# Kernel tuning notes

Measured on AMD Instinct MI355X. Metric: run time of the kernel, lower is better.

Reference implementation:

```python
import jax, jax.numpy as jnp
import numpy as np

EPS = 1e-5

def _conv1x1(x, w):
    # x: (B, Cin, N, K), w: (Cout, Cin) -> (B, Cout, N, K)
    return jnp.einsum('oc,bcnk->bonk', w, x)

def _bn2d(x, gamma, beta):
    # eval-mode BN with running_mean=0, running_var=1 (fresh init)
    scale = gamma / jnp.sqrt(1.0 + EPS)
    return x * scale[None, :, None, None] + beta[None, :, None, None]

def setup_inputs() -> dict:
    key = jax.random.key(0)
    ks = jax.random.split(key, 10)
    B, Cin, N, K = 8, 64, 1024, 32
    Cout, M = 64, 8
    Cin2 = 2 * Cin  # kernel_input='w_neighbor'
    features = jax.random.normal(ks[0], (B, Cin, N, K), dtype=jnp.float32)
    points_xyz = jax.random.normal(ks[1], (B, 3, N, K), dtype=jnp.float32)
    # ScoreNet convs: mlp_channels [7,16,16,16,M]; first 3 have BN (no bias), last has bias
    w1 = jax.random.normal(ks[2], (16, 7), dtype=jnp.float32) * (2.0 / 7) ** 0.5
    w2 = jax.random.normal(ks[3], (16, 16), dtype=jnp.float32) * (2.0 / 16) ** 0.5
    w3 = jax.random.normal(ks[4], (16, 16), dtype=jnp.float32) * (2.0 / 16) ** 0.5
    w4 = jax.random.normal(ks[5], (M, 16), dtype=jnp.float32) * (2.0 / 16) ** 0.5
    b4 = jnp.zeros((M,), dtype=jnp.float32)
    g1 = jnp.ones((16,), jnp.float32); be1 = jnp.zeros((16,), jnp.float32)
    g2 = jnp.ones((16,), jnp.float32); be2 = jnp.zeros((16,), jnp.float32)
    g3 = jnp.ones((16,), jnp.float32); be3 = jnp.zeros((16,), jnp.float32)
    # weight bank: kaiming_normal on (M, 2Cin, Cout) -> stored as (2Cin, M, Cout)
    wb = jax.random.normal(ks[6], (Cin2, M, Cout), dtype=jnp.float32) * (2.0 / Cin2) ** 0.5
    bn_g = jnp.ones((Cout,), jnp.float32); bn_b = jnp.zeros((Cout,), jnp.float32)
    return dict(features=features, points_xyz=points_xyz,
                w1=w1, g1=g1, be1=be1, w2=w2, g2=g2, be2=be2,
                w3=w3, g3=g3, be3=be3, w4=w4, b4=b4,
                weight_bank=wb, bn_g=bn_g, bn_b=bn_b)

def reference(features, points_xyz, w1, g1, be1, w2, g2, be2, w3, g3, be3,
              w4, b4, weight_bank, bn_g, bn_b):
    B, Cin, N, K = features.shape
    M = weight_bank.shape[1]
    # kernel_input = 'w_neighbor': concat(feat - center, feat) -> (B, 2Cin, N, K)
    center_f = features[..., :1]
    feat = jnp.concatenate([features - center_f, features], axis=1)
    # scorenet input = 'w_neighbor_dist': (center_xyz, xyz_diff, dist) -> (B, 7, N, K)
    center_xyz = jnp.broadcast_to(points_xyz[..., :1], points_xyz.shape)
    xyz_diff = points_xyz - center_xyz
    dist = jnp.sqrt(jnp.sum(xyz_diff * xyz_diff, axis=1, keepdims=True))
    xyz_feats = jnp.concatenate([center_xyz, xyz_diff, dist], axis=1)
    h = jax.nn.relu(_bn2d(_conv1x1(xyz_feats, w1), g1, be1))
    h = jax.nn.relu(_bn2d(_conv1x1(h, w2), g2, be2))
    h = jax.nn.relu(_bn2d(_conv1x1(h, w3), g3, be3))
    s = _conv1x1(h, w4) + b4[None, :, None, None]  # (B, M, N, K)
    scores = jax.nn.softmax(s, axis=1)
    scores = jnp.transpose(scores, (0, 2, 3, 1))  # (B, N, K, M)
    # matmul with weight bank then score-weighted sum over kernels, fused via einsum
    # original: (B,N,K,2Cin)@(2Cin,M*Cout) -> (B,N,K,M,Cout); sum_m scores * . -> (B,N,K,Cout)
    new_features = jnp.einsum('bcnk,cmo,bnkm->bonk', feat, weight_bank, scores)
    # BN2d (eval, fresh stats) + ReLU
    new_features = jax.nn.relu(_bn2d(new_features, bn_g, bn_b))
    return new_features
```

## Files before the change

kernel.cpp:

```cpp
#include <hip/hip_runtime.h>
#include <hip/hip_bf16.h>

typedef _Float16 f16;
typedef __attribute__((ext_vector_type(2))) _Float16 f16x2;
typedef __attribute__((ext_vector_type(8))) _Float16 f16x8;
typedef __attribute__((ext_vector_type(16))) float f32x16;

#define BNSCL 0.9999950000375f

__global__ __launch_bounds__(256) void k_scores(
    const float* __restrict__ xyz,
    const float* __restrict__ w1, const float* __restrict__ g1, const float* __restrict__ be1,
    const float* __restrict__ w2, const float* __restrict__ g2, const float* __restrict__ be2,
    const float* __restrict__ w3, const float* __restrict__ g3, const float* __restrict__ be3,
    const float* __restrict__ w4, const float* __restrict__ b4,
    const float* __restrict__ wb, f16* __restrict__ wbtA,
    f16* __restrict__ scores)
{
    __shared__ float lw[856];
    const int tid = threadIdx.x;

    if (blockIdx.x < 256) {
        int idx = blockIdx.x * 256 + tid;
        int j    = idx & 7;
        int lane = (idx >> 3) & 63;
        int ks   = (idx >> 9) & 63;
        int ot   = idx >> 15;
        int cp   = ks * 2 + (lane >> 5);
        int o    = ot * 32 + (lane & 31);
        wbtA[idx] = (f16)wb[(cp * 8 + j) * 64 + o];
    }

    if (tid < 112) lw[tid] = w1[tid];
    lw[112 + tid] = w2[tid];
    lw[368 + tid] = w3[tid];
    if (tid < 128) lw[624 + tid] = w4[tid];
    if (tid < 8)   lw[752 + tid] = b4[tid];
    if (tid < 16) {
        lw[760 + tid] = g1[tid] * BNSCL;  lw[776 + tid] = be1[tid];
        lw[792 + tid] = g2[tid] * BNSCL;  lw[808 + tid] = be2[tid];
        lw[824 + tid] = g3[tid] * BNSCL;  lw[840 + tid] = be3[tid];
    }
    __syncthreads();

    float in7[2][7], h1[2][16], h2[2][16], s[2][8];

#pragma unroll
    for (int q = 0; q < 2; ++q) {
        int g = blockIdx.x * 512 + q * 256 + tid;
        int b = g >> 15;
        int p = g & 32767;
        int pc = p & ~31;
        const float* xb = xyz + (size_t)b * 98304;
        float cx = xb[pc], cy = xb[32768 + pc], cz = xb[65536 + pc];
        float dx = xb[p] - cx, dy = xb[32768 + p] - cy, dz = xb[65536 + p] - cz;
        in7[q][0] = cx; in7[q][1] = cy; in7[q][2] = cz;
        in7[q][3] = dx; in7[q][4] = dy; in7[q][5] = dz;
        in7[q][6] = sqrtf(dx * dx + dy * dy + dz * dz);
    }

#pragma unroll
    for (int o = 0; o < 16; ++o) {
        float a0 = 0.f, a1 = 0.f;
#pragma unroll
        for (int c = 0; c < 7; ++c) {
            float w = lw[o * 7 + c];
            a0 += w * in7[0][c]; a1 += w * in7[1][c];
        }
        float gs = lw[760 + o], bb = lw[776 + o];
        h1[0][o] = fmaxf(a0 * gs + bb, 0.f);
        h1[1][o] = fmaxf(a1 * gs + bb, 0.f);
    }
#pragma unroll
    for (int o = 0; o < 16; ++o) {
        float a0 = 0.f, a1 = 0.f;
#pragma unroll
        for (int c = 0; c < 16; ++c) {
            float w = lw[112 + o * 16 + c];
            a0 += w * h1[0][c]; a1 += w * h1[1][c];
        }
        float gs = lw[792 + o], bb = lw[808 + o];
        h2[0][o] = fmaxf(a0 * gs + bb, 0.f);
        h2[1][o] = fmaxf(a1 * gs + bb, 0.f);
    }
#pragma unroll
    for (int o = 0; o < 16; ++o) {
        float a0 = 0.f, a1 = 0.f;
#pragma unroll
        for (int c = 0; c < 16; ++c) {
            float w = lw[368 + o * 16 + c];
            a0 += w * h2[0][c]; a1 += w * h2[1][c];
        }
        float gs = lw[824 + o], bb = lw[840 + o];
        h1[0][o] = fmaxf(a0 * gs + bb, 0.f);
        h1[1][o] = fmaxf(a1 * gs + bb, 0.f);
    }
#pragma unroll
    for (int o = 0; o < 8; ++o) {
        float bb = lw[752 + o];
        float a0 = bb, a1 = bb;
#pragma unroll
        for (int c = 0; c < 16; ++c) {
            float w = lw[624 + o * 16 + c];
            a0 += w * h1[0][c]; a1 += w * h1[1][c];
        }
        s[0][o] = a0; s[1][o] = a1;
    }

#pragma unroll
    for (int q = 0; q < 2; ++q) {
        int g = blockIdx.x * 512 + q * 256 + tid;
        float mx = s[q][0];
#pragma unroll
        for (int i = 1; i < 8; ++i) mx = fmaxf(mx, s[q][i]);
        float sum = 0.f;
#pragma unroll
        for (int i = 0; i < 8; ++i) { s[q][i] = __expf(s[q][i] - mx); sum += s[q][i]; }
        float inv = 1.f / sum;
        f16x8 o8;
#pragma unroll
        for (int i = 0; i < 8; ++i) o8[i] = (f16)(s[q][i] * inv);
        *(f16x8*)(scores + (size_t)g * 8) = o8;
    }
}

__global__ __launch_bounds__(512, 4) void k_main(
    const float* __restrict__ feat,
    const f16* __restrict__ scores,
    const f16* __restrict__ wbtA,
    const float* __restrict__ bn_g, const float* __restrict__ bn_b,
    float* __restrict__ out)
{
    __shared__ __align__(16) f16 lwb[32768];

    const int tid  = threadIdx.x;
    const int lane = tid & 63;
    const int wave = tid >> 6;
    const int l31  = lane & 31;
    const int lh   = lane >> 5;

    const int ot = blockIdx.x >> 9;
    const int g  = blockIdx.x & 511;
    const int pblock = g * 512;
    const int b    = pblock >> 15;
    const int pt0  = (pblock & 32767) + wave * 64;
    const int pc0  = pt0 + l31;
    const int pc1  = pc0 + 32;

    const f16* src = wbtA + ((size_t)ot << 15);
#pragma unroll
    for (int it = 0; it < 8; ++it) {
        int idx = it * 512 + tid;
        *(int4*)&lwb[idx << 3] = *(const int4*)&src[idx << 3];
    }
    __syncthreads();

    const float* fb = feat + (size_t)b * 2097152;

    const int gpt = pblock + wave * 64 + l31;
    f16x8 sv0 = *(const f16x8*)(scores + (size_t)gpt * 8);
    f16x8 sv1 = *(const f16x8*)(scores + (size_t)(gpt + 32) * 8);
    const f16x2 s0a = {sv0[0], sv0[1]}, s0b = {sv0[2], sv0[3]},
                s0c = {sv0[4], sv0[5]}, s0d = {sv0[6], sv0[7]};
    const f16x2 s1a = {sv1[0], sv1[1]}, s1b = {sv1[2], sv1[3]},
                s1c = {sv1[4], sv1[5]}, s1d = {sv1[6], sv1[7]};

    f32x16 acc0 = {}, acc1 = {};

    const f16* Alds = lwb + (lane << 3);

#pragma unroll 2
    for (int kk = 0; kk < 32; ++kk) {
        const float* fr = fb + ((size_t)(kk * 2 + lh) << 15);

        f16x8 aD = *(const f16x8*)(Alds + ((size_t)kk << 9));
        f16x8 aR = *(const f16x8*)(Alds + ((size_t)(kk + 32) << 9));

        float fv0 = fr[pc0], fv1 = fr[pc1];
        float fc0 = fr[pt0], fc1 = fr[pt0 + 32];

        f16 hR0 = (f16)fv0,          hR1 = (f16)fv1;
        f16 hD0 = (f16)(fv0 - fc0),  hD1 = (f16)(fv1 - fc1);
        f16x2 fR0 = {hR0, hR0}, fR1 = {hR1, hR1};
        f16x2 fD0 = {hD0, hD0}, fD1 = {hD1, hD1};

        f16x2 d0a = fD0 * s0a, d0b = fD0 * s0b, d0c = fD0 * s0c, d0d = fD0 * s0d;
        f16x2 d1a = fD1 * s1a, d1b = fD1 * s1b, d1c = fD1 * s1c, d1d = fD1 * s1d;
        f16x2 r0a = fR0 * s0a, r0b = fR0 * s0b, r0c = fR0 * s0c, r0d = fR0 * s0d;
        f16x2 r1a = fR1 * s1a, r1b = fR1 * s1b, r1c = fR1 * s1c, r1d = fR1 * s1d;

        f16x8 bD0 = {d0a[0],d0a[1],d0b[0],d0b[1],d0c[0],d0c[1],d0d[0],d0d[1]};
        f16x8 bD1 = {d1a[0],d1a[1],d1b[0],d1b[1],d1c[0],d1c[1],d1d[0],d1d[1]};
        f16x8 bR0 = {r0a[0],r0a[1],r0b[0],r0b[1],r0c[0],r0c[1],r0d[0],r0d[1]};
        f16x8 bR1 = {r1a[0],r1a[1],r1b[0],r1b[1],r1c[0],r1c[1],r1d[0],r1d[1]};

        acc0 = __builtin_amdgcn_mfma_f32_32x32x16_f16(aD, bD0, acc0, 0, 0, 0);
        acc1 = __builtin_amdgcn_mfma_f32_32x32x16_f16(aD, bD1, acc1, 0, 0, 0);
        acc0 = __builtin_amdgcn_mfma_f32_32x32x16_f16(aR, bR0, acc0, 0, 0, 0);
        acc1 = __builtin_amdgcn_mfma_f32_32x32x16_f16(aR, bR1, acc1, 0, 0, 0);
    }

#pragma unroll
    for (int q = 0; q < 2; ++q) {
        int pcol = (q == 0) ? pc0 : pc1;
        const f32x16& a = (q == 0) ? acc0 : acc1;
#pragma unroll
        for (int r = 0; r < 16; ++r) {
            int o = ot * 32 + (r & 3) + ((r >> 2) << 3) + (lh << 2);
            float v = a[r];
            v = v * (bn_g[o] * BNSCL) + bn_b[o];
            v = fmaxf(v, 0.f);
            out[((size_t)(b * 64 + o) << 15) + pcol] = v;
        }
    }
}

extern "C" void kernel_launch(void* const* d_in, const int* in_sizes, int n_in,
                              void* d_out, int out_size, void* d_ws, size_t ws_size,
                              hipStream_t stream)
{
    const float* features = (const float*)d_in[0];
    const float* xyz      = (const float*)d_in[1];
    const float* w1  = (const float*)d_in[2];
    const float* g1  = (const float*)d_in[3];
    const float* be1 = (const float*)d_in[4];
    const float* w2  = (const float*)d_in[5];
    const float* g2  = (const float*)d_in[6];
    const float* be2 = (const float*)d_in[7];
    const float* w3  = (const float*)d_in[8];
    const float* g3  = (const float*)d_in[9];
    const float* be3 = (const float*)d_in[10];
    const float* w4  = (const float*)d_in[11];
    const float* b4  = (const float*)d_in[12];
    const float* wb  = (const float*)d_in[13];
    const float* bn_g = (const float*)d_in[14];
    const float* bn_b = (const float*)d_in[15];

    f16* scores = (f16*)d_ws;
    f16* wbtA   = (f16*)((char*)d_ws + (4u << 20));

    k_scores<<<512, 256, 0, stream>>>(xyz, w1, g1, be1, w2, g2, be2,
                                      w3, g3, be3, w4, b4, wb, wbtA, scores);
    k_main<<<1024, 512, 0, stream>>>(features, scores, wbtA, bn_g, bn_b,
                                     (float*)d_out);
}
```

Measured before the change: 180.3 us.

## Fold weight-bank halves and precompute per-center correction via separate GEMM

The concat of (feat - center, feat) is rewritten algebraically. The two weight-bank halves are summed into one folded weight, and the center term is precomputed once per point group as a small GEMM (G = -center·W_diff) in a new kernel. The main kernel now runs half the K dimension, computes all 64 output channels per block instead of splitting by channel tile, and reads features only once. A final MFMA applies the correction with the scores. This halves the main MFMA work and the feature reads, at the cost of an extra launch, the G workspace traffic, and extra fp16 rounding on the summed weights.

```diff
diff --git a/kernel.cpp b/kernel.cpp
--- a/kernel.cpp
+++ b/kernel.cpp
@@ -7,6 +7,7 @@
 typedef __attribute__((ext_vector_type(16))) float f32x16;
 
 #define BNSCL 0.9999950000375f
+
 
 __global__ __launch_bounds__(256) void k_scores(
     const float* __restrict__ xyz,
@@ -14,21 +15,33 @@
     const float* __restrict__ w2, const float* __restrict__ g2, const float* __restrict__ be2,
     const float* __restrict__ w3, const float* __restrict__ g3, const float* __restrict__ be3,
     const float* __restrict__ w4, const float* __restrict__ b4,
-    const float* __restrict__ wb, f16* __restrict__ wbtA,
+    const float* __restrict__ wb, f16* __restrict__ wpf, f16* __restrict__ wdb,
     f16* __restrict__ scores)
 {
     __shared__ float lw[856];
     const int tid = threadIdx.x;
-
-    if (blockIdx.x < 256) {
-        int idx = blockIdx.x * 256 + tid;
+    const int bx  = blockIdx.x;
+
+    if (bx < 256) {
+        int idx  = bx * 256 + tid;
         int j    = idx & 7;
         int lane = (idx >> 3) & 63;
-        int ks   = (idx >> 9) & 63;
-        int ot   = idx >> 15;
-        int cp   = ks * 2 + (lane >> 5);
+        int ks   = (idx >> 9) & 31;
+        int ot   = idx >> 14;
+        int c    = ks * 2 + (lane >> 5);
         int o    = ot * 32 + (lane & 31);
-        wbtA[idx] = (f16)wb[(cp * 8 + j) * 64 + o];
+        float v  = wb[(c * 8 + j) * 64 + o] + wb[((c + 64) * 8 + j) * 64 + o];
+        wpf[idx] = (f16)v;
+    } else if (bx < 384) {
+        int idx  = (bx - 256) * 256 + tid;
+        int j    = idx & 7;
+        int lane = (idx >> 3) & 63;
+        int s    = (idx >> 9) & 3;
+        int T    = idx >> 11;
+        int om   = T * 32 + (lane & 31);
+        int o    = om >> 3, m = om & 7;
+        int c    = s * 16 + (lane >> 5) * 8 + j;
+        wdb[idx] = (f16)(-wb[(c * 8 + m) * 64 + o]);
     }
 
     if (tid < 112) lw[tid] = w1[tid];
@@ -47,7 +60,7 @@
 
 #pragma unroll
     for (int q = 0; q < 2; ++q) {
-        int g = blockIdx.x * 512 + q * 256 + tid;
+        int g = bx * 512 + q * 256 + tid;
         int b = g >> 15;
         int p = g & 32767;
         int pc = p & ~31;
@@ -109,7 +122,7 @@
 
 #pragma unroll
     for (int q = 0; q < 2; ++q) {
-        int g = blockIdx.x * 512 + q * 256 + tid;
+        int g = bx * 512 + q * 256 + tid;
         float mx = s[q][0];
 #pragma unroll
         for (int i = 1; i < 8; ++i) mx = fmaxf(mx, s[q][i]);
@@ -124,10 +137,57 @@
     }
 }
 
+__global__ __launch_bounds__(256) void k_gprep(
+    const float* __restrict__ feat,
+    const f16* __restrict__ wdb,
+    f16* __restrict__ G)
+{
+    __shared__ f16 fc16[32 * 64];
+
+    const int tid = threadIdx.x;
+    const int blk = blockIdx.x;
+    const int b   = blk >> 5;
+    const int nb  = (blk & 31) * 32;
+    const float* fb = feat + (size_t)b * 2097152 + (size_t)nb * 32;
+
+#pragma unroll
+    for (int it = 0; it < 8; ++it) {
+        int idx = it * 256 + tid;
+        int c = idx >> 5, g = idx & 31;
+        float v = fb[(size_t)c * 32768 + g * 32];
+        int cb = c >> 3, j = c & 7;
+        fc16[g * 64 + ((cb ^ (g & 7)) * 8) + j] = (f16)v;
+    }
+    __syncthreads();
+
+    const int lane = tid & 63, wave = tid >> 6;
+    const int l31  = lane & 31, lh = lane >> 5;
+    const int gbase = blk * 32;
+
+#pragma unroll
+    for (int tt = 0; tt < 4; ++tt) {
+        int T = wave * 4 + tt;
+        f32x16 acc = {};
+#pragma unroll
+        for (int s = 0; s < 4; ++s) {
+            int cb = s * 2 + lh;
+            f16x8 af = *(const f16x8*)&fc16[l31 * 64 + ((cb ^ (l31 & 7)) * 8)];
+            f16x8 bf = *(const f16x8*)&wdb[(((T * 4 + s) * 64) + lane) * 8];
+            acc = __builtin_amdgcn_mfma_f32_32x32x16_f16(af, bf, acc, 0, 0, 0);
+        }
+#pragma unroll
+        for (int r = 0; r < 16; ++r) {
+            int grow = (r & 3) + 8 * (r >> 2) + 4 * lh;
+            G[(size_t)(gbase + grow) * 512 + T * 32 + l31] = (f16)acc[r];
+        }
+    }
+}
+
 __global__ __launch_bounds__(512, 4) void k_main(
     const float* __restrict__ feat,
     const f16* __restrict__ scores,
-    const f16* __restrict__ wbtA,
+    const f16* __restrict__ wpf,
+    const f16* __restrict__ G,
     const float* __restrict__ bn_g, const float* __restrict__ bn_b,
     float* __restrict__ out)
 {
@@ -139,19 +199,18 @@
     const int l31  = lane & 31;
     const int lh   = lane >> 5;
 
-    const int ot = blockIdx.x >> 9;
-    const int g  = blockIdx.x & 511;
-    const int pblock = g * 512;
+    const int pblock = blockIdx.x * 512;
     const int b    = pblock >> 15;
     const int pt0  = (pblock & 32767) + wave * 64;
     const int pc0  = pt0 + l31;
     const int pc1  = pc0 + 32;
-
-    const f16* src = wbtA + ((size_t)ot << 15);
-#pragma unroll
-    for (int it = 0; it < 8; ++it) {
+    const int grp0 = (pblock + wave * 64) >> 5;
+    const int grp1 = grp0 + 1;
+
+#pragma unroll
+    for (int it = 0; it < 16; ++it) {
         int idx = it * 512 + tid;
-        *(int4*)&lwb[idx << 3] = *(const int4*)&src[idx << 3];
+        *(int4*)&lwb[idx << 3] = *(const int4*)&wpf[idx << 3];
     }
     __syncthreads();
 
@@ -165,52 +224,60 @@
     const f16x2 s1a = {sv1[0], sv1[1]}, s1b = {sv1[2], sv1[3]},
                 s1c = {sv1[4], sv1[5]}, s1d = {sv1[6], sv1[7]};
 
-    f32x16 acc0 = {}, acc1 = {};
-
-    const f16* Alds = lwb + (lane << 3);
-
-#pragma unroll 2
+    f32x16 acc00 = {}, acc01 = {}, acc10 = {}, acc11 = {};
+
+    const float* f0 = fb + ((size_t)lh << 15);
+
+#pragma unroll 4
     for (int kk = 0; kk < 32; ++kk) {
-        const float* fr = fb + ((size_t)(kk * 2 + lh) << 15);
-
-        f16x8 aD = *(const f16x8*)(Alds + ((size_t)kk << 9));
-        f16x8 aR = *(const f16x8*)(Alds + ((size_t)(kk + 32) << 9));
-
-        float fv0 = fr[pc0], fv1 = fr[pc1];
-        float fc0 = fr[pt0], fc1 = fr[pt0 + 32];
-
-        f16 hR0 = (f16)fv0,          hR1 = (f16)fv1;
-        f16 hD0 = (f16)(fv0 - fc0),  hD1 = (f16)(fv1 - fc1);
-        f16x2 fR0 = {hR0, hR0}, fR1 = {hR1, hR1};
-        f16x2 fD0 = {hD0, hD0}, fD1 = {hD1, hD1};
-
-        f16x2 d0a = fD0 * s0a, d0b = fD0 * s0b, d0c = fD0 * s0c, d0d = fD0 * s0d;
-        f16x2 d1a = fD1 * s1a, d1b = fD1 * s1b, d1c = fD1 * s1c, d1d = fD1 * s1d;
-        f16x2 r0a = fR0 * s0a, r0b = fR0 * s0b, r0c = fR0 * s0c, r0d = fR0 * s0d;
-        f16x2 r1a = fR1 * s1a, r1b = fR1 * s1b, r1c = fR1 * s1c, r1d = fR1 * s1d;
-
-        f16x8 bD0 = {d0a[0],d0a[1],d0b[0],d0b[1],d0c[0],d0c[1],d0d[0],d0d[1]};
-        f16x8 bD1 = {d1a[0],d1a[1],d1b[0],d1b[1],d1c[0],d1c[1],d1d[0],d1d[1]};
-        f16x8 bR0 = {r0a[0],r0a[1],r0b[0],r0b[1],r0c[0],r0c[1],r0d[0],r0d[1]};
-        f16x8 bR1 = {r1a[0],r1a[1],r1b[0],r1b[1],r1c[0],r1c[1],r1d[0],r1d[1]};
-
-        acc0 = __builtin_amdgcn_mfma_f32_32x32x16_f16(aD, bD0, acc0, 0, 0, 0);
-        acc1 = __builtin_amdgcn_mfma_f32_32x32x16_f16(aD, bD1, acc1, 0, 0, 0);
-        acc0 = __builtin_amdgcn_mfma_f32_32x32x16_f16(aR, bR0, acc0, 0, 0, 0);
-        acc1 = __builtin_amdgcn_mfma_f32_32x32x16_f16(aR, bR1, acc1, 0, 0, 0);
+        f16x8 a0 = *(const f16x8*)&lwb[((0 * 32 + kk) * 64 + lane) * 8];
+        f16x8 a1 = *(const f16x8*)&lwb[((1 * 32 + kk) * 64 + lane) * 8];
+
+        int off = kk << 16;
+        float fv0 = f0[off + pc0];
+        float fv1 = f0[off + pc1];
+
+        f16 h0 = (f16)fv0, h1 = (f16)fv1;
+        f16x2 f0v = {h0, h0}, f1v = {h1, h1};
+        f16x2 p0a = f0v * s0a, p0b = f0v * s0b, p0c = f0v * s0c, p0d = f0v * s0d;
+        f16x2 p1a = f1v * s1a, p1b = f1v * s1b, p1c = f1v * s1c, p1d = f1v * s1d;
+        f16x8 bv0 = {p0a[0],p0a[1],p0b[0],p0b[1],p0c[0],p0c[1],p0d[0],p0d[1]};
+        f16x8 bv1 = {p1a[0],p1a[1],p1b[0],p1b[1],p1c[0],p1c[1],p1d[0],p1d[1]};
+
+        acc00 = __builtin_amdgcn_mfma_f32_32x32x16_f16(a0, bv0, acc00, 0, 0, 0);
+        acc01 = __builtin_amdgcn_mfma_f32_32x32x16_f16(a1, bv0, acc01, 0, 0, 0);
+        acc10 = __builtin_amdgcn_mfma_f32_32x32x16_f16(a0, bv1, acc10, 0, 0, 0);
+        acc11 = __builtin_amdgcn_mfma_f32_32x32x16_f16(a1, bv1, acc11, 0, 0, 0);
+    }
+
+    {
+        const f16x8 z = {};
+        f16x8 g00 = *(const f16x8*)&G[(size_t)grp0 * 512 + (0 * 32 + l31) * 8];
+        f16x8 g01 = *(const f16x8*)&G[(size_t)grp0 * 512 + (1 * 32 + l31) * 8];
+        f16x8 g10 = *(const f16x8*)&G[(size_t)grp1 * 512 + (0 * 32 + l31) * 8];
+        f16x8 g11 = *(const f16x8*)&G[(size_t)grp1 * 512 + (1 * 32 + l31) * 8];
+        if (lh) { g00 = z; g01 = z; g10 = z; g11 = z; }
+        acc00 = __builtin_amdgcn_mfma_f32_32x32x16_f16(g00, sv0, acc00, 0, 0, 0);
+        acc01 = __builtin_amdgcn_mfma_f32_32x32x16_f16(g01, sv0, acc01, 0, 0, 0);
+        acc10 = __builtin_amdgcn_mfma_f32_32x32x16_f16(g10, sv1, acc10, 0, 0, 0);
+        acc11 = __builtin_amdgcn_mfma_f32_32x32x16_f16(g11, sv1, acc11, 0, 0, 0);
     }
 
 #pragma unroll
     for (int q = 0; q < 2; ++q) {
         int pcol = (q == 0) ? pc0 : pc1;
-        const f32x16& a = (q == 0) ? acc0 : acc1;
-#pragma unroll
-        for (int r = 0; r < 16; ++r) {
-            int o = ot * 32 + (r & 3) + ((r >> 2) << 3) + (lh << 2);
-            float v = a[r];
-            v = v * (bn_g[o] * BNSCL) + bn_b[o];
-            v = fmaxf(v, 0.f);
-            out[((size_t)(b * 64 + o) << 15) + pcol] = v;
+#pragma unroll
+        for (int ot = 0; ot < 2; ++ot) {
+            const f32x16& a = (q == 0) ? (ot == 0 ? acc00 : acc01)
+                                       : (ot == 0 ? acc10 : acc11);
+#pragma unroll
+            for (int r = 0; r < 16; ++r) {
+                int o = ot * 32 + (r & 3) + ((r >> 2) << 3) + (lh << 2);
+                float v = a[r];
+                v = v * (bn_g[o] * BNSCL) + bn_b[o];
+                v = fmaxf(v, 0.f);
+                out[((size_t)(b * 64 + o) << 15) + pcol] = v;
+            }
         }
     }
 }
@@ -236,11 +303,15 @@
     const float* bn_g = (const float*)d_in[14];
     const float* bn_b = (const float*)d_in[15];
 
-    f16* scores = (f16*)d_ws;
-    f16* wbtA   = (f16*)((char*)d_ws + (4u << 20));
+    char* ws = (char*)d_ws;
+    f16* scores = (f16*)ws;
+    f16* G      = (f16*)(ws + (4u  << 20));
+    f16* wpf    = (f16*)(ws + (12u << 20));
+    f16* wdb    = (f16*)(ws + (12u << 20) + (256u << 10));
 
     k_scores<<<512, 256, 0, stream>>>(xyz, w1, g1, be1, w2, g2, be2,
-                                      w3, g3, be3, w4, b4, wb, wbtA, scores);
-    k_main<<<1024, 512, 0, stream>>>(features, scores, wbtA, bn_g, bn_b,
-                                     (float*)d_out);
+                                      w3, g3, be3, w4, b4, wb, wpf, wdb, scores);
+    k_gprep<<<256, 256, 0, stream>>>(features, wdb, G);
+    k_main<<<512, 512, 0, stream>>>(features, scores, wpf, G, bn_g, bn_b,
+                                    (float*)d_out);
 }
```

New measurement: 189.0 us. 4.8% more time.
